# Kernel optimization log

Hardware: AMD Instinct MI355X
Metric: run time of the kernel (lower is better)

The kernel has to match this reference:

```python
import jax, jax.numpy as jnp
import numpy as np

N_NODES = 20000
N_EDGES = 500000


def setup_inputs() -> dict:
    key = jax.random.key(0)
    ks = jax.random.split(key, 12)
    s = 0.05  # small init scale for numerical sanity
    return {
        "z": jax.random.normal(ks[0], (N_NODES, 64), jnp.float32),
        "edge_index": jax.random.randint(ks[1], (2, N_EDGES), 0, N_NODES, jnp.int64),
        "celline_feats": jax.random.normal(ks[2], (N_NODES, 4), jnp.float32),
        "esm_repr": jax.random.normal(ks[3], (N_NODES, 320), jnp.float32),
        "mlp_w1": jax.random.normal(ks[4], (4, 64), jnp.float32) * s,
        "mlp_b1": jnp.zeros((64,), jnp.float32),
        "mlp_w2": jax.random.normal(ks[5], (64, 32), jnp.float32) * s,
        "mlp_b2": jnp.zeros((32,), jnp.float32),
        "mlp_w3": jax.random.normal(ks[6], (32, 16), jnp.float32) * s,
        "mlp_b3": jnp.zeros((16,), jnp.float32),
        "fc1_w": jax.random.normal(ks[7], (800, 400), jnp.float32) * s,
        "fc1_b": jnp.zeros((400,), jnp.float32),
        "fc2_w": jax.random.normal(ks[8], (400, 200), jnp.float32) * s,
        "fc2_b": jnp.zeros((200,), jnp.float32),
        "fc3_w": jax.random.normal(ks[9], (200, 100), jnp.float32) * s,
        "fc3_b": jnp.zeros((100,), jnp.float32),
        "fc4_w": jax.random.normal(ks[10], (100, 1), jnp.float32) * s,
        "fc4_b": jnp.zeros((1,), jnp.float32),
    }


def reference(z, edge_index, celline_feats, esm_repr,
              mlp_w1, mlp_b1, mlp_w2, mlp_b2, mlp_w3, mlp_b3,
              fc1_w, fc1_b, fc2_w, fc2_b, fc3_w, fc3_b, fc4_w, fc4_b):
    # cell_line_spec_mlp: 4 -> 64 -> 32 -> 16 (relu, relu, linear)
    m = jax.nn.relu(celline_feats @ mlp_w1 + mlp_b1)
    m = jax.nn.relu(m @ mlp_w2 + mlp_b2)
    m = m @ mlp_w3 + mlp_b3                       # [N, 16]
    # augment node embeddings: [N, 64+16+320] = [N, 400]
    zc = jnp.concatenate([z, m, esm_repr], axis=1)
    # gather endpoints, concat pair features: [E, 800]
    x = jnp.concatenate([zc[edge_index[0]], zc[edge_index[1]]], axis=1)
    # classifier MLP (dropout = identity in eval mode)
    x = jax.nn.relu(x @ fc1_w + fc1_b)
    x = jax.nn.relu(x @ fc2_w + fc2_b)
    x = jax.nn.relu(x @ fc3_w + fc3_b)
    x = x @ fc4_w + fc4_b                          # [E, 1]
    return jnp.squeeze(x, axis=-1)                 # [E]
```

## Files before the change

kernel.cpp:

```cpp
#include <hip/hip_runtime.h>


using u16    = unsigned short;
using f16    = _Float16;
using f16x8  = __attribute__((ext_vector_type(8))) f16;
using f32x4  = __attribute__((ext_vector_type(4))) float;
using f32x16 = __attribute__((ext_vector_type(16))) float;
using i32x4  = __attribute__((ext_vector_type(4))) int;

#define NN   20000
#define NNP  20032
#define KD   416
#define NE   500000

#define W1F_ELEMS (50*13*512)
#define W2F_ELEMS (7*26*512)
#define W3F_ELEMS (4*14*512)
#define F4_ELEMS  128
#define PREP_TOT  (W1F_ELEMS + W2F_ELEMS + W3F_ELEMS + F4_ELEMS)

#define ZC_BLOCKS   (NNP / 4)
#define PREP_BLOCKS ((PREP_TOT + 255) / 256)

__device__ __forceinline__ u16 f2h(float f) {
  f16 h = (f16)f;
  return __builtin_bit_cast(u16, h);
}

__device__ __forceinline__ int cvt_pk_f16(float lo, float hi) {
  int r;
  asm("v_cvt_pkrtz_f16_f32 %0, %1, %2" : "=v"(r) : "v"(lo), "v"(hi));
  return r;
}

__device__ __forceinline__ int pk_addrelu(int p, int q) {
  int r;
  asm("v_pk_add_f16 %0, %1, %2\n\t"
      "v_pk_max_f16 %0, %0, 0"
      : "=&v"(r) : "v"(p), "v"(q));
  return r;
}

__device__ __forceinline__ void gl_lds16(const u16* g, u16* l) {
  __builtin_amdgcn_global_load_lds(
      (const __attribute__((address_space(1))) unsigned int*)g,
      (__attribute__((address_space(3))) unsigned int*)l, 16, 0, 0);
}

__global__ __launch_bounds__(256) void prep_fused(
    const float* __restrict__ z, const float* __restrict__ cell,
    const float* __restrict__ esm,
    const float* __restrict__ w1, const float* __restrict__ b1,
    const float* __restrict__ w2, const float* __restrict__ b2,
    const float* __restrict__ w3, const float* __restrict__ b3,
    u16* __restrict__ zc,
    const float* __restrict__ fc1, const float* __restrict__ fc1b,
    const float* __restrict__ fc2, const float* __restrict__ fc2b,
    const float* __restrict__ fc3, const float* __restrict__ fc3b,
    const float* __restrict__ fc4,
    u16* __restrict__ W1f, u16* __restrict__ W2f, u16* __restrict__ W3f,
    float* __restrict__ fc4wp)
{
  __shared__ float h1s[4][64];
  __shared__ float h2s[4][32];
  __shared__ float ms[4][16];

  if (blockIdx.x < ZC_BLOCKS) {
    int tid = threadIdx.x, g = tid >> 6, t = tid & 63;
    int i = blockIdx.x * 4 + g;
    bool real = (i < NN);
    float c0 = 0, c1 = 0, c2 = 0, c3 = 0;
    if (real) {
      c0 = cell[(size_t)i * 4 + 0]; c1 = cell[(size_t)i * 4 + 1];
      c2 = cell[(size_t)i * 4 + 2]; c3 = cell[(size_t)i * 4 + 3];
    }
    float h = b1[t] + c0 * w1[t] + c1 * w1[64 + t] + c2 * w1[128 + t] + c3 * w1[192 + t];
    h1s[g][t] = fmaxf(h, 0.f);
    __syncthreads();
    if (t < 32) {
      float acc = b2[t];
      #pragma unroll 8
      for (int j = 0; j < 64; j++) acc += h1s[g][j] * w2[j * 32 + t];
      h2s[g][t] = fmaxf(acc, 0.f);
    }
    __syncthreads();
    if (t < 16) {
      float acc = b3[t];
      #pragma unroll 8
      for (int j = 0; j < 32; j++) acc += h2s[g][j] * w3[j * 16 + t];
      ms[g][t] = acc;
    }
    __syncthreads();
    u16* row = zc + (size_t)i * KD;
    for (int k = t; k < KD; k += 64) {
      float v = 0.f;
      if (real) {
        if (k < 64)       v = z[(size_t)i * 64 + k];
        else if (k < 80)  v = ms[g][k - 64];
        else if (k < 400) v = esm[(size_t)i * 320 + (k - 80)];
        else if (k == 400) v = 1.0f;
      }
      row[k] = f2h(v);
    }
    return;
  }

  int idx = (blockIdx.x - ZC_BLOCKS) * 256 + threadIdx.x;
  if (idx < W1F_ELEMS) {
    int j = idx & 7, l = (idx >> 3) & 63, t = idx >> 9;
    int kb = t % 13, g = t / 13;
    int n = g * 16 + (l & 15);
    int k = kb * 32 + (l >> 4) * 8 + j;
    float v = 0.f;
    if (k < 400) v = (n < 400) ? fc1[(size_t)k * 400 + n]
                               : fc1[(size_t)(400 + k) * 400 + (n - 400)];
    else if (k == 400 && n < 400) v = fc1b[n];
    W1f[idx] = f2h(v);
  } else if (idx < W1F_ELEMS + W2F_ELEMS) {
    int r = idx - W1F_ELEMS;
    int j = r & 7, l = (r >> 3) & 63, t = r >> 9;
    int kb = t % 26, nt = t / 26;
    int n = nt * 32 + (l & 31);
    int k = kb * 16 + (l >> 5) * 8 + j;
    float v = 0.f;
    if (n < 200) {
      if (k < 400) v = fc2[(size_t)k * 200 + n];
      else if (k == 400) v = fc2b[n];
    }
    W2f[r] = f2h(v);
  } else if (idx < W1F_ELEMS + W2F_ELEMS + W3F_ELEMS) {
    int r = idx - (W1F_ELEMS + W2F_ELEMS);
    int j = r & 7, l = (r >> 3) & 63, t = r >> 9;
    int kb = t % 14, nt = t / 14;
    int n = nt * 32 + (l & 31);
    int k = kb * 16 + (l >> 5) * 8 + j;
    float v = 0.f;
    if (n < 100) {
      if (k < 200) v = fc3[(size_t)k * 100 + n];
      else if (k == 200) v = fc3b[n];
    }
    W3f[r] = f2h(v);
  } else if (idx < PREP_TOT) {
    int r = idx - (W1F_ELEMS + W2F_ELEMS + W3F_ELEMS);
    fc4wp[r] = (r < 100) ? fc4[r] : 0.f;
  }
}

__global__ __launch_bounds__(256) void node_gemm(
    const u16* __restrict__ zc, const u16* __restrict__ W1f,
    u16* __restrict__ PQ)
{
  int tid = threadIdx.x, w = tid >> 6, l = tid & 63, lm = l & 15, quad = l >> 4;
  int mbase = blockIdx.x * 128 + w * 32;

  int ra = mbase + lm;       if (ra > NNP - 1) ra = NNP - 1;
  int rb = mbase + 16 + lm;  if (rb > NNP - 1) rb = NNP - 1;
  f16x8 a0[13], a1[13];
  const u16* arow0 = zc + (size_t)ra * KD + quad * 8;
  const u16* arow1 = zc + (size_t)rb * KD + quad * 8;
  #pragma unroll
  for (int kb = 0; kb < 13; kb++) {
    a0[kb] = *(const f16x8*)(arow0 + kb * 32);
    a1[kb] = *(const f16x8*)(arow1 + kb * 32);
  }

  for (int nt = 0; nt < 10; nt++) {
    int g = blockIdx.y * 10 + nt;
    int ncol = g * 16 + lm;
    const u16* bbase = W1f + ((size_t)g * 13 * 64 + l) * 8;
    f32x4 acc0 = {0.f, 0.f, 0.f, 0.f};
    f32x4 acc1 = {0.f, 0.f, 0.f, 0.f};
    #pragma unroll
    for (int kb = 0; kb < 13; kb++) {
      f16x8 b = *(const f16x8*)(bbase + (size_t)kb * 512);
      acc0 = __builtin_amdgcn_mfma_f32_16x16x32_f16(a0[kb], b, acc0, 0, 0, 0);
      acc1 = __builtin_amdgcn_mfma_f32_16x16x32_f16(a1[kb], b, acc1, 0, 0, 0);
    }
    #pragma unroll
    for (int r = 0; r < 4; r++) {
      int row0 = mbase + quad * 4 + r;
      int row1 = row0 + 16;
      if (row0 < NNP) PQ[(size_t)row0 * 800 + ncol] = f2h(acc0[r]);
      if (row1 < NNP) PQ[(size_t)row1 * 800 + ncol] = f2h(acc1[r]);
    }
  }
}

__global__ __launch_bounds__(256, 2) void edge_kernel(
    const u16* __restrict__ PQ, const u16* __restrict__ W2f,
    const u16* __restrict__ W3f, const float* __restrict__ fc4wp,
    const float* __restrict__ fc4b,
    const int* __restrict__ ei, float* __restrict__ out)
{
  __shared__ __align__(16) u16 wsm[2][26 * 512];

  int tid = threadIdx.x, w = tid >> 6, l = tid & 63;
  int c = l & 31, h = l >> 5;
  int e = blockIdx.x * 128 + w * 32 + c;
  int ec = e < NE ? e : NE - 1;
  int s = ei[ec], d = ei[NE + ec];
  const u16* prow = PQ + (size_t)s * 800 + h * 8;
  const u16* qrow = PQ + (size_t)d * 800 + 400 + h * 8;

  for (int kb = w; kb < 26; kb += 4)
    gl_lds16(W2f + ((size_t)kb * 64 + l) * 8, &wsm[0][kb * 512]);

  i32x4 h1i[25];
  #pragma unroll
  for (int kb = 0; kb < 25; kb++) {
    i32x4 pv = *(const i32x4*)(prow + kb * 16);
    i32x4 qv = *(const i32x4*)(qrow + kb * 16);
    i32x4 r;
    #pragma unroll
    for (int j2 = 0; j2 < 4; j2++) r[j2] = pk_addrelu(pv[j2], qv[j2]);
    h1i[kb] = r;
  }
  i32x4 bias1 = {0, 0, 0, 0};
  if (h == 0) bias1[0] = 0x3C00;

  __syncthreads();

  int p2[7][8];
  #pragma unroll
  for (int nt = 0; nt < 7; nt++) {
    int cur = nt & 1;
    if (nt < 6) {
      for (int kb = w; kb < 26; kb += 4)
        gl_lds16(W2f + (((size_t)(nt + 1) * 26 + kb) * 64 + l) * 8,
                 &wsm[cur ^ 1][kb * 512]);
    } else {
      for (int kb = w; kb < 13; kb += 4)
        gl_lds16(W3f + ((size_t)kb * 64 + l) * 8, &wsm[cur ^ 1][kb * 512]);
    }
    f32x16 acc = {0.f,0.f,0.f,0.f,0.f,0.f,0.f,0.f,0.f,0.f,0.f,0.f,0.f,0.f,0.f,0.f};
    __builtin_amdgcn_s_setprio(1);
    #pragma unroll
    for (int kb = 0; kb < 25; kb++) {
      f16x8 a = *(const f16x8*)&wsm[cur][kb * 512 + l * 8];
      acc = __builtin_amdgcn_mfma_f32_32x32x16_f16(
          a, __builtin_bit_cast(f16x8, h1i[kb]), acc, 0, 0, 0);
    }
    {
      f16x8 a = *(const f16x8*)&wsm[cur][25 * 512 + l * 8];
      acc = __builtin_amdgcn_mfma_f32_32x32x16_f16(
          a, __builtin_bit_cast(f16x8, bias1), acc, 0, 0, 0);
    }
    __builtin_amdgcn_s_setprio(0);
    #pragma unroll
    for (int q = 0; q < 8; q++)
      p2[nt][q] = cvt_pk_f16(fmaxf(acc[2 * q], 0.f), fmaxf(acc[2 * q + 1], 0.f));
    __syncthreads();
  }

  i32x4 b2f[13];
  #pragma unroll
  for (int kb3 = 0; kb3 < 13; kb3++) {
    int nt = kb3 >> 1;
    i32x4 f;
    #pragma unroll
    for (int jj = 0; jj < 4; jj++) {
      int q0 = (jj & 1) + 4 * (kb3 & 1);
      if (jj < 2) {
        int x = __shfl_xor(p2[nt][q0 + 2], 32);
        f[jj] = h ? x : p2[nt][q0];
      } else {
        int y = __shfl_xor(p2[nt][q0], 32);
        f[jj] = h ? p2[nt][q0 + 2] : y;
      }
    }
    if (kb3 == 12 && h) f[0] |= 0x3C00;
    b2f[kb3] = f;
  }

  float osum = 0.f;
  #pragma unroll
  for (int nt3 = 0; nt3 < 4; nt3++) {
    int cur = (7 + nt3) & 1;
    if (nt3 < 3) {
      for (int kb = w; kb < 13; kb += 4)
        gl_lds16(W3f + (((size_t)(nt3 + 1) * 14 + kb) * 64 + l) * 8,
                 &wsm[cur ^ 1][kb * 512]);
    }
    f32x16 acc = {0.f,0.f,0.f,0.f,0.f,0.f,0.f,0.f,0.f,0.f,0.f,0.f,0.f,0.f,0.f,0.f};
    __builtin_amdgcn_s_setprio(1);
    #pragma unroll
    for (int kb3 = 0; kb3 < 13; kb3++) {
      f16x8 a = *(const f16x8*)&wsm[cur][kb3 * 512 + l * 8];
      acc = __builtin_amdgcn_mfma_f32_32x32x16_f16(
          a, __builtin_bit_cast(f16x8, b2f[kb3]), acc, 0, 0, 0);
    }
    __builtin_amdgcn_s_setprio(0);
    #pragma unroll
    for (int r = 0; r < 16; r++) {
      int rho = (r & 3) + 8 * (r >> 2) + 4 * h + 32 * nt3;
      osum += fmaxf(acc[r], 0.f) * fc4wp[rho];
    }
    if (nt3 < 3) __syncthreads();
  }
  osum += __shfl_xor(osum, 32);
  if (h == 0 && e < NE) out[e] = osum + fc4b[0];
}

extern "C" void kernel_launch(void* const* d_in, const int* in_sizes, int n_in,
                              void* d_out, int out_size, void* d_ws, size_t ws_size,
                              hipStream_t stream) {
  (void)in_sizes; (void)n_in; (void)out_size; (void)ws_size;
  const float* z    = (const float*)d_in[0];
  const int*   ei   = (const int*)d_in[1];
  const float* cell = (const float*)d_in[2];
  const float* esm  = (const float*)d_in[3];
  const float* w1   = (const float*)d_in[4];
  const float* b1   = (const float*)d_in[5];
  const float* w2   = (const float*)d_in[6];
  const float* b2   = (const float*)d_in[7];
  const float* w3   = (const float*)d_in[8];
  const float* b3   = (const float*)d_in[9];
  const float* fc1w = (const float*)d_in[10];
  const float* fc1b = (const float*)d_in[11];
  const float* fc2w = (const float*)d_in[12];
  const float* fc2b = (const float*)d_in[13];
  const float* fc3w = (const float*)d_in[14];
  const float* fc3b = (const float*)d_in[15];
  const float* fc4w = (const float*)d_in[16];
  const float* fc4b = (const float*)d_in[17];
  float* out = (float*)d_out;

  u16* zc  = (u16*)d_ws;
  u16* PQ  = zc  + (size_t)NNP * KD;
  u16* W1f = PQ  + (size_t)NNP * 800;
  u16* W2f = W1f + W1F_ELEMS;
  u16* W3f = W2f + W2F_ELEMS;
  float* fc4wp = (float*)(W3f + W3F_ELEMS);

  prep_fused<<<ZC_BLOCKS + PREP_BLOCKS, 256, 0, stream>>>(
      z, cell, esm, w1, b1, w2, b2, w3, b3, zc,
      fc1w, fc1b, fc2w, fc2b, fc3w, fc3b, fc4w, W1f, W2f, W3f, fc4wp);
  node_gemm<<<dim3((NNP + 127) / 128, 5), 256, 0, stream>>>(zc, W1f, PQ);
  edge_kernel<<<(NE + 127) / 128, 256, 0, stream>>>(PQ, W2f, W3f, fc4wp, fc4b, ei, out);
}
```

Measured before the change: 356.8 us.

## Triple-buffer weight staging in edge kernel with explicit vmcnt waits

Replaces the double-buffered LDS weight staging for the fc2/fc3 tiles with a three-buffer pipeline that prefetches two tiles ahead. Each wave now loads a contiguous range of k-blocks, and __syncthreads is replaced by raw s_barrier plus per-wave s_waitcnt vmcnt counts, so each wave waits only for the loads it issued that are actually needed. The aim is to hide global-to-LDS latency behind the MFMA work and to avoid the full memory drain that __syncthreads forces. In exchange LDS use rises by half, which may limit occupancy, and the hand-tuned vmcnt counts are fragile.

```diff
diff --git a/kernel.cpp b/kernel.cpp
--- a/kernel.cpp
+++ b/kernel.cpp
@@ -186,13 +186,34 @@
   }
 }
 
+
+#define STAGE_FC2(t, b) { \
+    int s_ = (w < 2) ? 7 * w : 14 + 6 * (w - 2); \
+    int c_ = (w < 2) ? 7 : 6; \
+    for (int kb = s_; kb < s_ + c_; kb++) \
+      gl_lds16(W2f + (((size_t)(t) * 26 + kb) * 64 + l) * 8, &wsm[b][kb * 512]); }
+
+#define STAGE_FC3(u, b) { \
+    int s_ = (w < 2) ? 4 * w : 8 + 3 * (w - 2); \
+    int c_ = (w < 2) ? 4 : 3; \
+    for (int kb = s_; kb < s_ + c_; kb++) \
+      gl_lds16(W3f + (((size_t)(u) * 14 + kb) * 64 + l) * 8, &wsm[b][kb * 512]); }
+
+#define SYNC(WLO, WHI) \
+    if (w < 2) asm volatile("s_waitcnt vmcnt(" #WLO ")" ::: "memory"); \
+    else       asm volatile("s_waitcnt vmcnt(" #WHI ")" ::: "memory"); \
+    __builtin_amdgcn_s_barrier(); \
+    __builtin_amdgcn_sched_barrier(0);
+
+#define PHASE_TOP() __builtin_amdgcn_s_barrier();
+
 __global__ __launch_bounds__(256, 2) void edge_kernel(
     const u16* __restrict__ PQ, const u16* __restrict__ W2f,
     const u16* __restrict__ W3f, const float* __restrict__ fc4wp,
     const float* __restrict__ fc4b,
     const int* __restrict__ ei, float* __restrict__ out)
 {
-  __shared__ __align__(16) u16 wsm[2][26 * 512];
+  __shared__ __align__(16) u16 wsm[3][26 * 512];
 
   int tid = threadIdx.x, w = tid >> 6, l = tid & 63;
   int c = l & 31, h = l >> 5;
@@ -202,8 +223,8 @@
   const u16* prow = PQ + (size_t)s * 800 + h * 8;
   const u16* qrow = PQ + (size_t)d * 800 + 400 + h * 8;
 
-  for (int kb = w; kb < 26; kb += 4)
-    gl_lds16(W2f + ((size_t)kb * 64 + l) * 8, &wsm[0][kb * 512]);
+  STAGE_FC2(0, 0);
+  STAGE_FC2(1, 1);
 
   i32x4 h1i[25];
   #pragma unroll
@@ -218,39 +239,32 @@
   i32x4 bias1 = {0, 0, 0, 0};
   if (h == 0) bias1[0] = 0x3C00;
 
-  __syncthreads();
-
   int p2[7][8];
-  #pragma unroll
-  for (int nt = 0; nt < 7; nt++) {
-    int cur = nt & 1;
-    if (nt < 6) {
-      for (int kb = w; kb < 26; kb += 4)
-        gl_lds16(W2f + (((size_t)(nt + 1) * 26 + kb) * 64 + l) * 8,
-                 &wsm[cur ^ 1][kb * 512]);
-    } else {
-      for (int kb = w; kb < 13; kb += 4)
-        gl_lds16(W3f + ((size_t)kb * 64 + l) * 8, &wsm[cur ^ 1][kb * 512]);
-    }
-    f32x16 acc = {0.f,0.f,0.f,0.f,0.f,0.f,0.f,0.f,0.f,0.f,0.f,0.f,0.f,0.f,0.f,0.f};
-    __builtin_amdgcn_s_setprio(1);
-    #pragma unroll
-    for (int kb = 0; kb < 25; kb++) {
-      f16x8 a = *(const f16x8*)&wsm[cur][kb * 512 + l * 8];
-      acc = __builtin_amdgcn_mfma_f32_32x32x16_f16(
-          a, __builtin_bit_cast(f16x8, h1i[kb]), acc, 0, 0, 0);
-    }
-    {
-      f16x8 a = *(const f16x8*)&wsm[cur][25 * 512 + l * 8];
-      acc = __builtin_amdgcn_mfma_f32_32x32x16_f16(
-          a, __builtin_bit_cast(f16x8, bias1), acc, 0, 0, 0);
-    }
-    __builtin_amdgcn_s_setprio(0);
-    #pragma unroll
-    for (int q = 0; q < 8; q++)
-      p2[nt][q] = cvt_pk_f16(fmaxf(acc[2 * q], 0.f), fmaxf(acc[2 * q + 1], 0.f));
-    __syncthreads();
-  }
+
+  #define FC2_TILE(nt, b) { \
+    f32x16 acc = {0.f,0.f,0.f,0.f,0.f,0.f,0.f,0.f,0.f,0.f,0.f,0.f,0.f,0.f,0.f,0.f}; \
+    __builtin_amdgcn_s_setprio(1); \
+    _Pragma("unroll") \
+    for (int kb = 0; kb < 25; kb++) { \
+      f16x8 a = *(const f16x8*)&wsm[b][kb * 512 + l * 8]; \
+      acc = __builtin_amdgcn_mfma_f32_32x32x16_f16( \
+          a, __builtin_bit_cast(f16x8, h1i[kb]), acc, 0, 0, 0); \
+    } \
+    { f16x8 a = *(const f16x8*)&wsm[b][25 * 512 + l * 8]; \
+      acc = __builtin_amdgcn_mfma_f32_32x32x16_f16( \
+          a, __builtin_bit_cast(f16x8, bias1), acc, 0, 0, 0); } \
+    __builtin_amdgcn_s_setprio(0); \
+    _Pragma("unroll") \
+    for (int q = 0; q < 8; q++) \
+      p2[nt][q] = cvt_pk_f16(fmaxf(acc[2 * q], 0.f), fmaxf(acc[2 * q + 1], 0.f)); }
+
+  PHASE_TOP(); STAGE_FC2(2, 2); SYNC(14, 12); FC2_TILE(0, 0);
+  PHASE_TOP(); STAGE_FC2(3, 0); SYNC(14, 12); FC2_TILE(1, 1);
+  PHASE_TOP(); STAGE_FC2(4, 1); SYNC(14, 12); FC2_TILE(2, 2);
+  PHASE_TOP(); STAGE_FC2(5, 2); SYNC(14, 12); FC2_TILE(3, 0);
+  PHASE_TOP(); STAGE_FC2(6, 0); SYNC(14, 12); FC2_TILE(4, 1);
+  PHASE_TOP(); STAGE_FC3(0, 1); SYNC(11,  9); FC2_TILE(5, 2);
+  PHASE_TOP(); STAGE_FC3(1, 2); SYNC( 8,  6); FC2_TILE(6, 0);
 
   i32x4 b2f[13];
   #pragma unroll
@@ -273,30 +287,27 @@
   }
 
   float osum = 0.f;
-  #pragma unroll
-  for (int nt3 = 0; nt3 < 4; nt3++) {
-    int cur = (7 + nt3) & 1;
-    if (nt3 < 3) {
-      for (int kb = w; kb < 13; kb += 4)
-        gl_lds16(W3f + (((size_t)(nt3 + 1) * 14 + kb) * 64 + l) * 8,
-                 &wsm[cur ^ 1][kb * 512]);
-    }
-    f32x16 acc = {0.f,0.f,0.f,0.f,0.f,0.f,0.f,0.f,0.f,0.f,0.f,0.f,0.f,0.f,0.f,0.f};
-    __builtin_amdgcn_s_setprio(1);
-    #pragma unroll
-    for (int kb3 = 0; kb3 < 13; kb3++) {
-      f16x8 a = *(const f16x8*)&wsm[cur][kb3 * 512 + l * 8];
-      acc = __builtin_amdgcn_mfma_f32_32x32x16_f16(
-          a, __builtin_bit_cast(f16x8, b2f[kb3]), acc, 0, 0, 0);
-    }
-    __builtin_amdgcn_s_setprio(0);
-    #pragma unroll
-    for (int r = 0; r < 16; r++) {
-      int rho = (r & 3) + 8 * (r >> 2) + 4 * h + 32 * nt3;
-      osum += fmaxf(acc[r], 0.f) * fc4wp[rho];
-    }
-    if (nt3 < 3) __syncthreads();
-  }
+
+  #define FC3_TILE(u, b) { \
+    f32x16 acc = {0.f,0.f,0.f,0.f,0.f,0.f,0.f,0.f,0.f,0.f,0.f,0.f,0.f,0.f,0.f,0.f}; \
+    __builtin_amdgcn_s_setprio(1); \
+    _Pragma("unroll") \
+    for (int kb3 = 0; kb3 < 13; kb3++) { \
+      f16x8 a = *(const f16x8*)&wsm[b][kb3 * 512 + l * 8]; \
+      acc = __builtin_amdgcn_mfma_f32_32x32x16_f16( \
+          a, __builtin_bit_cast(f16x8, b2f[kb3]), acc, 0, 0, 0); \
+    } \
+    __builtin_amdgcn_s_setprio(0); \
+    _Pragma("unroll") \
+    for (int r = 0; r < 16; r++) { \
+      int rho = (r & 3) + 8 * (r >> 2) + 4 * h + 32 * (u); \
+      osum += fmaxf(acc[r], 0.f) * fc4wp[rho]; } }
+
+  PHASE_TOP(); STAGE_FC3(2, 0); SYNC( 8,  6); FC3_TILE(0, 1);
+  PHASE_TOP(); STAGE_FC3(3, 1); SYNC( 8,  6); FC3_TILE(1, 2);
+  PHASE_TOP();                  SYNC( 4,  3); FC3_TILE(2, 0);
+  PHASE_TOP();                  SYNC( 0,  0); FC3_TILE(3, 1);
+
   osum += __shfl_xor(osum, 32);
   if (h == 0 && e < NE) out[e] = osum + fc4b[0];
 }
```

Result: no change. 361.7 us (+1.4%).

## Compute cell-line MLP per thread and copy node rows with wave-per-row layout

Applied to the files above, without the earlier changes.

Rebuilds the node-feature build stage so each thread evaluates the whole 4→64→32→16 cell-line MLP for one node in registers, instead of a 64-thread group per node with three barriers. Results go to shared memory as fp16. Each wave then copies 64 rows of z, MLP output, esm and bias padding into the fp16 zc buffer. The aim is fewer barriers and far fewer blocks for the build part of the prep kernel. In exchange it launches only about 79 build blocks, which risks poor GPU occupancy, and the large per-thread register arrays may spill. Row stores stay coalesced across the wave, but the row loop is serial per wave.

```diff
diff --git a/kernel.cpp b/kernel.cpp
--- a/kernel.cpp
+++ b/kernel.cpp
@@ -19,8 +19,8 @@
 #define F4_ELEMS  128
 #define PREP_TOT  (W1F_ELEMS + W2F_ELEMS + W3F_ELEMS + F4_ELEMS)
 
-#define ZC_BLOCKS   (NNP / 4)
-#define PREP_BLOCKS ((PREP_TOT + 255) / 256)
+#define BUILD_BLOCKS ((NNP + 255) / 256)
+#define PREP_BLOCKS  ((PREP_TOT + 255) / 256)
 
 __device__ __forceinline__ u16 f2h(float f) {
   f16 h = (f16)f;
@@ -61,51 +61,66 @@
     u16* __restrict__ W1f, u16* __restrict__ W2f, u16* __restrict__ W3f,
     float* __restrict__ fc4wp)
 {
-  __shared__ float h1s[4][64];
-  __shared__ float h2s[4][32];
-  __shared__ float ms[4][16];
-
-  if (blockIdx.x < ZC_BLOCKS) {
-    int tid = threadIdx.x, g = tid >> 6, t = tid & 63;
-    int i = blockIdx.x * 4 + g;
+  __shared__ u16 ms[256][16];
+
+  if (blockIdx.x < BUILD_BLOCKS) {
+    int tid = threadIdx.x;
+    int i = blockIdx.x * 256 + tid;
     bool real = (i < NN);
-    float c0 = 0, c1 = 0, c2 = 0, c3 = 0;
-    if (real) {
-      c0 = cell[(size_t)i * 4 + 0]; c1 = cell[(size_t)i * 4 + 1];
-      c2 = cell[(size_t)i * 4 + 2]; c3 = cell[(size_t)i * 4 + 3];
-    }
-    float h = b1[t] + c0 * w1[t] + c1 * w1[64 + t] + c2 * w1[128 + t] + c3 * w1[192 + t];
-    h1s[g][t] = fmaxf(h, 0.f);
+    {
+      float c0 = 0, c1 = 0, c2 = 0, c3 = 0;
+      if (real) {
+        c0 = cell[(size_t)i * 4 + 0]; c1 = cell[(size_t)i * 4 + 1];
+        c2 = cell[(size_t)i * 4 + 2]; c3 = cell[(size_t)i * 4 + 3];
+      }
+      float h1[64];
+      #pragma unroll
+      for (int j = 0; j < 64; j++)
+        h1[j] = fmaxf(b1[j] + c0 * w1[j] + c1 * w1[64 + j]
+                            + c2 * w1[128 + j] + c3 * w1[192 + j], 0.f);
+      float h2[32];
+      #pragma unroll
+      for (int t2 = 0; t2 < 32; t2++) h2[t2] = b2[t2];
+      #pragma unroll
+      for (int j = 0; j < 64; j++) {
+        float hv = h1[j];
+        #pragma unroll
+        for (int t2 = 0; t2 < 32; t2++) h2[t2] += hv * w2[j * 32 + t2];
+      }
+      float m[16];
+      #pragma unroll
+      for (int t3 = 0; t3 < 16; t3++) m[t3] = b3[t3];
+      #pragma unroll
+      for (int j = 0; j < 32; j++) {
+        float hv = fmaxf(h2[j], 0.f);
+        #pragma unroll
+        for (int t3 = 0; t3 < 16; t3++) m[t3] += hv * w3[j * 16 + t3];
+      }
+      #pragma unroll
+      for (int t3 = 0; t3 < 16; t3++) ms[tid][t3] = real ? f2h(m[t3]) : (u16)0;
+    }
     __syncthreads();
-    if (t < 32) {
-      float acc = b2[t];
-      #pragma unroll 8
-      for (int j = 0; j < 64; j++) acc += h1s[g][j] * w2[j * 32 + t];
-      h2s[g][t] = fmaxf(acc, 0.f);
-    }
-    __syncthreads();
-    if (t < 16) {
-      float acc = b3[t];
-      #pragma unroll 8
-      for (int j = 0; j < 32; j++) acc += h2s[g][j] * w3[j * 16 + t];
-      ms[g][t] = acc;
-    }
-    __syncthreads();
-    u16* row = zc + (size_t)i * KD;
-    for (int k = t; k < KD; k += 64) {
-      float v = 0.f;
-      if (real) {
-        if (k < 64)       v = z[(size_t)i * 64 + k];
-        else if (k < 80)  v = ms[g][k - 64];
-        else if (k < 400) v = esm[(size_t)i * 320 + (k - 80)];
-        else if (k == 400) v = 1.0f;
-      }
-      row[k] = f2h(v);
+
+    int w = tid >> 6, t = tid & 63;
+    int base = blockIdx.x * 256;
+    for (int k = 0; k < 64; k++) {
+      int nn = base + w * 64 + k;
+      if (nn >= NNP) break;
+      bool rn = (nn < NN);
+      u16* row = zc + (size_t)nn * KD;
+      row[t] = rn ? f2h(z[(size_t)nn * 64 + t]) : (u16)0;
+      if (t < 16) row[64 + t] = ms[nn - base][t];
+      #pragma unroll
+      for (int cch = 0; cch < 5; cch++)
+        row[80 + cch * 64 + t] =
+            rn ? f2h(esm[(size_t)nn * 320 + cch * 64 + t]) : (u16)0;
+      if (t < 16)
+        row[400 + t] = (rn && t == 0) ? (u16)0x3C00 : (u16)0;
     }
     return;
   }
 
-  int idx = (blockIdx.x - ZC_BLOCKS) * 256 + threadIdx.x;
+  int idx = (blockIdx.x - BUILD_BLOCKS) * 256 + threadIdx.x;
   if (idx < W1F_ELEMS) {
     int j = idx & 7, l = (idx >> 3) & 63, t = idx >> 9;
     int kb = t % 13, g = t / 13;
@@ -332,7 +347,7 @@
   u16* W3f = W2f + W2F_ELEMS;
   float* fc4wp = (float*)(W3f + W3F_ELEMS);
 
-  prep_fused<<<ZC_BLOCKS + PREP_BLOCKS, 256, 0, stream>>>(
+  prep_fused<<<BUILD_BLOCKS + PREP_BLOCKS, 256, 0, stream>>>(
       z, cell, esm, w1, b1, w2, b2, w3, b3, zc,
       fc1w, fc1b, fc2w, fc2b, fc3w, fc3b, fc4w, W1f, W2f, W3f, fc4wp);
   node_gemm<<<dim3((NNP + 127) / 128, 5), 256, 0, stream>>>(zc, W1f, PQ);
```

Result: slower. 434.7 us (+21.8%).

## Bucket-sort edges by source node and swizzle edge blocks for gather locality

Applied to the files above, without the earlier changes.

Adds a histogram, scan and scatter pass that reorders edges into buckets of 128 source nodes, so edge blocks gather PQ rows with better cache locality. The edge kernel reads the sorted src/dst/original-index arrays, writes results back through the original index, and remaps block IDs so that consecutive launched blocks take work from eight separate regions of the sorted list. The extra passes add several small kernel launches, global atomics and extra memory traffic in exchange for fewer cache misses on the irregular gathers.

```diff
diff --git a/kernel.cpp b/kernel.cpp
--- a/kernel.cpp
+++ b/kernel.cpp
@@ -12,6 +12,9 @@
 #define NNP  20032
 #define KD   416
 #define NE   500000
+#define NEP  500736
+#define GRID_E 3912
+#define NB   157
 
 #define W1F_ELEMS (50*13*512)
 #define W2F_ELEMS (7*26*512)
@@ -21,6 +24,7 @@
 
 #define ZC_BLOCKS   (NNP / 4)
 #define PREP_BLOCKS ((PREP_TOT + 255) / 256)
+#define HIST_BLOCKS ((NE + 1023) / 1024)
 
 __device__ __forceinline__ u16 f2h(float f) {
   f16 h = (f16)f;
@@ -59,11 +63,13 @@
     const float* __restrict__ fc3, const float* __restrict__ fc3b,
     const float* __restrict__ fc4,
     u16* __restrict__ W1f, u16* __restrict__ W2f, u16* __restrict__ W3f,
-    float* __restrict__ fc4wp)
+    float* __restrict__ fc4wp,
+    const int* __restrict__ ei, int* __restrict__ hist)
 {
   __shared__ float h1s[4][64];
   __shared__ float h2s[4][32];
   __shared__ float ms[4][16];
+  __shared__ int lh[NB];
 
   if (blockIdx.x < ZC_BLOCKS) {
     int tid = threadIdx.x, g = tid >> 6, t = tid & 63;
@@ -102,6 +108,22 @@
       }
       row[k] = f2h(v);
     }
+    return;
+  }
+
+  if (blockIdx.x >= ZC_BLOCKS + PREP_BLOCKS) {
+    int tid = threadIdx.x;
+    int base = (blockIdx.x - (ZC_BLOCKS + PREP_BLOCKS)) * 1024;
+    for (int i = tid; i < NB; i += 256) lh[i] = 0;
+    __syncthreads();
+    #pragma unroll
+    for (int k = 0; k < 4; k++) {
+      int e = base + k * 256 + tid;
+      if (e < NE) atomicAdd(&lh[ei[e] >> 7], 1);
+    }
+    __syncthreads();
+    for (int i = tid; i < NB; i += 256)
+      if (lh[i]) atomicAdd(&hist[i], lh[i]);
     return;
   }
 
@@ -146,6 +168,61 @@
   }
 }
 
+__global__ __launch_bounds__(256) void scan_pad(
+    const int* __restrict__ hist, int* __restrict__ cursor,
+    int* __restrict__ sq, int* __restrict__ dq, int* __restrict__ oq)
+{
+  __shared__ int h[NB];
+  __shared__ int cs[NB];
+  int t = threadIdx.x;
+  if (t < NB) h[t] = hist[t];
+  __syncthreads();
+  if (t == 0) {
+    int run = 0;
+    for (int b = 0; b < NB; b++) { cs[b] = run; run += h[b]; }
+  }
+  __syncthreads();
+  if (t < NB) cursor[t] = cs[t];
+  for (int i = NE + t; i < NEP; i += 256) {
+    sq[i] = 0; dq[i] = 0; oq[i] = 0x7FFFFFFF;
+  }
+}
+
+__global__ __launch_bounds__(256) void scatter_edges(
+    const int* __restrict__ ei, int* __restrict__ cursor,
+    int* __restrict__ sq, int* __restrict__ dq, int* __restrict__ oq)
+{
+  __shared__ int lh[NB];
+  __shared__ int lb[NB];
+  int t = threadIdx.x;
+  int base = blockIdx.x * 1024;
+  for (int i = t; i < NB; i += 256) lh[i] = 0;
+  __syncthreads();
+  int sv[4], dv[4], bv[4], rv[4];
+  bool val[4];
+  #pragma unroll
+  for (int k = 0; k < 4; k++) {
+    int e = base + k * 256 + t;
+    val[k] = (e < NE);
+    if (val[k]) {
+      sv[k] = ei[e]; dv[k] = ei[NE + e];
+      bv[k] = sv[k] >> 7;
+      rv[k] = atomicAdd(&lh[bv[k]], 1);
+    }
+  }
+  __syncthreads();
+  for (int i = t; i < NB; i += 256)
+    lb[i] = lh[i] ? atomicAdd(&cursor[i], lh[i]) : 0;
+  __syncthreads();
+  #pragma unroll
+  for (int k = 0; k < 4; k++) {
+    if (val[k]) {
+      int pos = lb[bv[k]] + rv[k];
+      sq[pos] = sv[k]; dq[pos] = dv[k]; oq[pos] = base + k * 256 + t;
+    }
+  }
+}
+
 __global__ __launch_bounds__(256) void node_gemm(
     const u16* __restrict__ zc, const u16* __restrict__ W1f,
     u16* __restrict__ PQ)
@@ -190,15 +267,17 @@
     const u16* __restrict__ PQ, const u16* __restrict__ W2f,
     const u16* __restrict__ W3f, const float* __restrict__ fc4wp,
     const float* __restrict__ fc4b,
-    const int* __restrict__ ei, float* __restrict__ out)
+    const int* __restrict__ sq, const int* __restrict__ dq,
+    const int* __restrict__ oq, float* __restrict__ out)
 {
   __shared__ __align__(16) u16 wsm[2][26 * 512];
 
   int tid = threadIdx.x, w = tid >> 6, l = tid & 63;
   int c = l & 31, h = l >> 5;
-  int e = blockIdx.x * 128 + w * 32 + c;
-  int ec = e < NE ? e : NE - 1;
-  int s = ei[ec], d = ei[NE + ec];
+  int bid = blockIdx.x;
+  int idx = (bid & 7) * (GRID_E / 8) + (bid >> 3);
+  int e = idx * 128 + w * 32 + c;
+  int s = sq[e], d = dq[e], oi = oq[e];
   const u16* prow = PQ + (size_t)s * 800 + h * 8;
   const u16* qrow = PQ + (size_t)d * 800 + 400 + h * 8;
 
@@ -298,7 +377,7 @@
     if (nt3 < 3) __syncthreads();
   }
   osum += __shfl_xor(osum, 32);
-  if (h == 0 && e < NE) out[e] = osum + fc4b[0];
+  if (h == 0 && oi < NE) out[oi] = osum + fc4b[0];
 }
 
 extern "C" void kernel_launch(void* const* d_in, const int* in_sizes, int n_in,
@@ -331,10 +410,20 @@
   u16* W2f = W1f + W1F_ELEMS;
   u16* W3f = W2f + W2F_ELEMS;
   float* fc4wp = (float*)(W3f + W3F_ELEMS);
-
-  prep_fused<<<ZC_BLOCKS + PREP_BLOCKS, 256, 0, stream>>>(
+  int* hist   = (int*)(fc4wp + 128);
+  int* cursor = hist + 160;
+  int* sq     = cursor + 160;
+  int* dq     = sq + NEP;
+  int* oq     = dq + NEP;
+
+  hipMemsetAsync(hist, 0, NB * sizeof(int), stream);
+  prep_fused<<<ZC_BLOCKS + PREP_BLOCKS + HIST_BLOCKS, 256, 0, stream>>>(
       z, cell, esm, w1, b1, w2, b2, w3, b3, zc,
-      fc1w, fc1b, fc2w, fc2b, fc3w, fc3b, fc4w, W1f, W2f, W3f, fc4wp);
+      fc1w, fc1b, fc2w, fc2b, fc3w, fc3b, fc4w, W1f, W2f, W3f, fc4wp,
+      ei, hist);
+  scan_pad<<<1, 256, 0, stream>>>(hist, cursor, sq, dq, oq);
+  scatter_edges<<<HIST_BLOCKS, 256, 0, stream>>>(ei, cursor, sq, dq, oq);
   node_gemm<<<dim3((NNP + 127) / 128, 5), 256, 0, stream>>>(zc, W1f, PQ);
-  edge_kernel<<<(NE + 127) / 128, 256, 0, stream>>>(PQ, W2f, W3f, fc4wp, fc4b, ei, out);
-}
+  edge_kernel<<<GRID_E, 256, 0, stream>>>(PQ, W2f, W3f, fc4wp, fc4b,
+                                          sq, dq, oq, out);
+}
```

New measurement: 370.2 us. 1.04x slower.
